# Optimization experiments

Measured on AMD Instinct MI355X. Metric: run time of the kernel, lower is better.

## Reference

```python
import jax, jax.numpy as jnp
import numpy as np

B, S, D, H, T = 64, 512, 1024, 1024, 9


def setup_inputs() -> dict:
    key = jax.random.key(0)
    ks = jax.random.split(key, 8)
    return {
        "input_": jax.random.normal(ks[0], (B, S, D), dtype=jnp.float32),
        "labels": jax.random.randint(ks[1], (B, S), 0, T),
        "attention_mask": jnp.ones((B, S), dtype=jnp.int32),
        # linear_1: input_dim -> hidden_dim (stored [in, out])
        "W1": (jax.random.normal(ks[2], (D, H), dtype=jnp.float32) * 0.02),
        "b1": jnp.zeros((H,), dtype=jnp.float32),
        # linear_2: hidden_dim -> tag_dim
        "W2": (jax.random.normal(ks[3], (H, T), dtype=jnp.float32) * 0.02),
        "b2": jnp.zeros((T,), dtype=jnp.float32),
        # torchcrf params: uniform(-0.1, 0.1)
        "start_trans": jax.random.uniform(ks[4], (T,), minval=-0.1, maxval=0.1),
        "end_trans": jax.random.uniform(ks[5], (T,), minval=-0.1, maxval=0.1),
        "trans": jax.random.uniform(ks[6], (T, T), minval=-0.1, maxval=0.1),
    }


def _crf_mean_llh(logits, tags, mask, start, end, trans):
    """torchcrf.CRF log-likelihood, reduction='mean'. logits [B,S,T]."""
    nb = logits.shape[0]
    em = jnp.transpose(logits, (1, 0, 2))          # [S,B,T] time-major
    tg = tags.T                                    # [S,B]
    m = mask.T.astype(logits.dtype)                # [S,B]
    bidx = jnp.arange(nb)

    # --- numerator: score of the gold path ---
    score0 = start[tg[0]] + em[0, bidx, tg[0]]

    def num_step(carry, x):
        score, last = carry
        em_t, tag_t, m_t = x
        score = score + (trans[last, tag_t] + em_t[bidx, tag_t]) * m_t
        last = jnp.where(m_t > 0, tag_t, last)
        return (score, last), None

    (score, last), _ = jax.lax.scan(num_step, (score0, tg[0]), (em[1:], tg[1:], m[1:]))
    score = score + end[last]

    # --- denominator: log-partition via logsumexp forward recurrence ---
    alpha0 = start[None, :] + em[0]                # [B,T]

    def part_step(alpha, x):
        em_t, m_t = x
        # [B, prev T, next T] semiring (log-sum-exp) matrix product
        nxt = jax.nn.logsumexp(alpha[:, :, None] + trans[None, :, :] + em_t[:, None, :], axis=1)
        alpha = jnp.where(m_t[:, None] > 0, nxt, alpha)
        return alpha, None

    alpha, _ = jax.lax.scan(part_step, alpha0, (em[1:], m[1:]))
    log_z = jax.nn.logsumexp(alpha + end[None, :], axis=1)

    return jnp.mean(score - log_z)


def reference(input_, labels, attention_mask, W1, b1, W2, b2, start_trans, end_trans, trans):
    # dropout layers are identity in eval mode
    h = input_ @ W1 + b1                           # [B,S,H]
    logits = h @ W2 + b2                           # [B,S,T]
    llh = _crf_mean_llh(logits, labels, attention_mask, start_trans, end_trans, trans)
    loss = -llh                                    # forward returns (-1*crf_llh, logits)
    return (loss, logits)
```

## Files before the change

### kernel.cpp

```cpp
#include <hip/hip_runtime.h>

#define BD 64
#define SD 512
#define DD 1024
#define HD 1024
#define TD 9
#define NSEG 8
#define SEGL 64
#define NEGI -1e30f

__device__ __forceinline__ float lse9(const float v[9]) {
    float m0 = fmaxf(v[0], v[1]);
    float m1 = fmaxf(v[2], v[3]);
    float m2 = fmaxf(v[4], v[5]);
    float m3 = fmaxf(v[6], v[7]);
    float mx = fmaxf(fmaxf(m0, m1), fmaxf(fmaxf(m2, m3), v[8]));
    float s = __expf(v[0] - mx) + __expf(v[1] - mx) + __expf(v[2] - mx)
            + __expf(v[3] - mx) + __expf(v[4] - mx) + __expf(v[5] - mx)
            + __expf(v[6] - mx) + __expf(v[7] - mx) + __expf(v[8] - mx);
    return mx + __logf(s);
}

__global__ __launch_bounds__(256) void k_w12(const float* __restrict__ W1,
                                             const float* __restrict__ b1,
                                             const float* __restrict__ W2,
                                             const float* __restrict__ b2,
                                             float* __restrict__ W12t,
                                             float* __restrict__ b12) {
    __shared__ float sh_w2[HD * TD];
    __shared__ float red[256 * TD];
    const int tid = threadIdx.x;
    const int d = blockIdx.x;

    for (int i = tid; i < HD * TD / 4; i += 256)
        ((float4*)sh_w2)[i] = ((const float4*)W2)[i];
    __syncthreads();

    const float* row = (d < DD) ? (W1 + (size_t)d * HD) : b1;
    float4 x = ((const float4*)row)[tid];

    float acc[TD];
#pragma unroll
    for (int t = 0; t < TD; t++) acc[t] = 0.f;
#pragma unroll
    for (int u = 0; u < 4; u++) {
        float xv = (&x.x)[u];
        int h = tid * 4 + u;
#pragma unroll
        for (int t = 0; t < TD; t++) acc[t] += xv * sh_w2[h * TD + t];
    }
#pragma unroll
    for (int t = 0; t < TD; t++) red[tid * TD + t] = acc[t];
    __syncthreads();

    if (tid < TD) {
        float s = 0.f;
        for (int i = 0; i < 256; i++) s += red[i * TD + tid];
        if (d < DD) W12t[tid * DD + d] = s;
        else        b12[tid] = s + b2[tid];
    }
}

__global__ __launch_bounds__(256) void k_gemm2(const float* __restrict__ X,
                                               const float* __restrict__ W12t,
                                               const float* __restrict__ b12,
                                               float* __restrict__ logits) {
    __shared__ float wt[TD][DD];
    __shared__ float bb[TD];

    for (int i = threadIdx.x; i < TD * DD / 4; i += 256)
        ((float4*)&wt[0][0])[i] = ((const float4*)W12t)[i];
    if (threadIdx.x < TD) bb[threadIdx.x] = b12[threadIdx.x];
    __syncthreads();

    const int wave = threadIdx.x >> 6;
    const int lane = threadIdx.x & 63;
    const int g = lane >> 3;
    const int l8 = lane & 7;
    const int row = blockIdx.x * 32 + wave * 8 + g;

    const float4* xr = (const float4*)(X + (size_t)row * DD);

    float acc[TD];
#pragma unroll
    for (int t = 0; t < TD; t++) acc[t] = 0.f;

#pragma unroll 4
    for (int k = 0; k < 32; k++) {
        int d4 = l8 + k * 8;
        float4 x = xr[d4];
#pragma unroll
        for (int t = 0; t < TD; t++) {
            float4 w = *(const float4*)&wt[t][d4 * 4];
            acc[t] += x.x * w.x + x.y * w.y + x.z * w.z + x.w * w.w;
        }
    }

#pragma unroll
    for (int t = 0; t < TD; t++) {
        float v = acc[t];
        v += __shfl_xor(v, 1);
        v += __shfl_xor(v, 2);
        v += __shfl_xor(v, 4);
        acc[t] = v;
    }

    float* out = logits + (size_t)row * TD;
    if (l8 < 8) out[l8] = acc[l8] + bb[l8];
    if (l8 == 0) out[8] = acc[8] + bb[8];
}

__global__ __launch_bounds__(256) void k_crf_seg(const float* __restrict__ logits,
                                                 const int* __restrict__ maskp,
                                                 const float* __restrict__ transp,
                                                 float* __restrict__ segP) {
    const int blk = blockIdx.x;
    const int b = blk >> 3, s = blk & 7;
    const int tid = threadIdx.x;

    __shared__ float tr[81];
    __shared__ float em[SEGL * 9];
    __shared__ int   mk[SEGL];
    __shared__ float bufA[32 * 81];
    __shared__ float bufB[16 * 81];

    const int t0 = s * SEGL + 1;

    for (int i = tid; i < SEGL * 9; i += 256) {
        int q = i / 9, j = i - q * 9;
        int t = t0 + q;
        em[i] = (t < SD) ? logits[((size_t)b * SD + t) * TD + j] : 0.f;
    }
    if (tid < SEGL) {
        int t = t0 + tid;
        mk[tid] = (t < SD) ? maskp[b * SD + t] : 0;
    }
    if (tid < 81) tr[tid] = transp[tid];
    __syncthreads();

    for (int e = tid; e < 32 * 81; e += 256) {
        int p = e / 81, r = e - p * 81;
        int i = r / 9, j = r - i * 9;
        int la = 2 * p, lb = 2 * p + 1;
        int mA = mk[la], mB = mk[lb];
        float out;
        if (mA && mB) {
            float v[9];
#pragma unroll
            for (int k = 0; k < 9; k++)
                v[k] = tr[i * 9 + k] + em[la * 9 + k] + tr[k * 9 + j];
            out = lse9(v) + em[lb * 9 + j];
        } else if (mA) {
            out = tr[r] + em[la * 9 + j];
        } else if (mB) {
            out = tr[r] + em[lb * 9 + j];
        } else {
            out = (i == j) ? 0.f : NEGI;
        }
        bufA[e] = out;
    }
    __syncthreads();

#define COMBINE(SRC, DST, NP)                                        \
    for (int e = tid; e < (NP) * 81; e += 256) {                     \
        int p = e / 81, r = e - p * 81;                              \
        int i = r / 9, j = r - i * 9;                                \
        const float* Am = (SRC) + (2 * p) * 81;                      \
        const float* Bm = (SRC) + (2 * p + 1) * 81;                  \
        float v[9];                                                  \
        _Pragma("unroll")                                            \
        for (int k = 0; k < 9; k++) v[k] = Am[i * 9 + k] + Bm[k * 9 + j]; \
        (DST)[e] = lse9(v);                                          \
    }                                                                \
    __syncthreads();

    COMBINE(bufA, bufB, 16)
    COMBINE(bufB, bufA, 8)
    COMBINE(bufA, bufB, 4)
    COMBINE(bufB, bufA, 2)

    if (tid < 81) {
        int i = tid / 9, j = tid - (tid / 9) * 9;
        float v[9];
#pragma unroll
        for (int k = 0; k < 9; k++) v[k] = bufA[i * 9 + k] + bufA[81 + k * 9 + j];
        segP[(size_t)blk * 81 + tid] = lse9(v);
    }
}

__global__ __launch_bounds__(256) void k_crf_fin(const float* __restrict__ logits,
                                                 const int* __restrict__ labels,
                                                 const int* __restrict__ maskp,
                                                 const float* __restrict__ startp,
                                                 const float* __restrict__ endp,
                                                 const float* __restrict__ transp,
                                                 const float* __restrict__ segP,
                                                 float* __restrict__ diff) {
    const int b = blockIdx.x;
    const int tid = threadIdx.x;

    __shared__ float S[8 * 81];
    __shared__ float A4[4 * 81];
    __shared__ float A2[2 * 81];
    __shared__ float P[81];
    __shared__ float finv[81];
    __shared__ float red[256];
    __shared__ int   redi[256];

    for (int i = tid; i < 8 * 81; i += 256) S[i] = segP[(size_t)b * 8 * 81 + i];
    __syncthreads();

    for (int e = tid; e < 4 * 81; e += 256) {
        int p = e / 81, r = e - p * 81;
        int i = r / 9, j = r - i * 9;
        const float* Am = S + (2 * p) * 81;
        const float* Bm = S + (2 * p + 1) * 81;
        float v[9];
#pragma unroll
        for (int k = 0; k < 9; k++) v[k] = Am[i * 9 + k] + Bm[k * 9 + j];
        A4[e] = lse9(v);
    }
    __syncthreads();

    for (int e = tid; e < 2 * 81; e += 256) {
        int p = e / 81, r = e - p * 81;
        int i = r / 9, j = r - i * 9;
        const float* Am = A4 + (2 * p) * 81;
        const float* Bm = A4 + (2 * p + 1) * 81;
        float v[9];
#pragma unroll
        for (int k = 0; k < 9; k++) v[k] = Am[i * 9 + k] + Bm[k * 9 + j];
        A2[e] = lse9(v);
    }
    __syncthreads();

    if (tid < 81) {
        int i = tid / 9, j = tid - (tid / 9) * 9;
        float v[9];
#pragma unroll
        for (int k = 0; k < 9; k++) v[k] = A2[i * 9 + k] + A2[81 + k * 9 + j];
        P[tid] = lse9(v);
    }
    __syncthreads();

    if (tid < 81) {
        int k = tid / 9, j = tid - (tid / 9) * 9;
        finv[tid] = startp[k] + logits[(size_t)b * SD * TD + k] + P[tid] + endp[j];
    }

    float part = 0.f;
    for (int t = 1 + tid; t < SD; t += 256) {
        if (maskp[b * SD + t]) {
            int tgp = labels[b * SD + t - 1];
            int tgc = labels[b * SD + t];
            part += transp[tgp * TD + tgc] + logits[((size_t)b * SD + t) * TD + tgc];
        }
    }
    int lastt = 0;
    for (int t = tid; t < SD; t += 256) {
        if (maskp[b * SD + t]) lastt = max(lastt, t);
    }
    red[tid] = part;
    redi[tid] = lastt;
    __syncthreads();

    if (tid < 64) {
        float p4 = red[tid] + red[tid + 64] + red[tid + 128] + red[tid + 192];
        int l4 = max(max(redi[tid], redi[tid + 64]), max(redi[tid + 128], redi[tid + 192]));
#pragma unroll
        for (int m = 1; m < 64; m <<= 1) {
            p4 += __shfl_xor(p4, m);
            l4 = max(l4, __shfl_xor(l4, m));
        }
        float v1 = finv[tid];
        float v2 = (tid + 64 < 81) ? finv[tid + 64] : NEGI;
        float mx = fmaxf(v1, v2);
#pragma unroll
        for (int m = 1; m < 64; m <<= 1) mx = fmaxf(mx, __shfl_xor(mx, m));
        float ssum = __expf(v1 - mx) + __expf(v2 - mx);
#pragma unroll
        for (int m = 1; m < 64; m <<= 1) ssum += __shfl_xor(ssum, m);
        float logz = mx + __logf(ssum);

        if (tid == 0) {
            int tg0 = labels[b * SD];
            int tgl = labels[b * SD + l4];
            float score = p4 + startp[tg0] + logits[(size_t)b * SD * TD + tg0] + endp[tgl];
            diff[b] = score - logz;
        }
    }
}

__global__ __launch_bounds__(64) void k_loss(const float* __restrict__ diff,
                                             float* __restrict__ out) {
    float v = (threadIdx.x < BD) ? diff[threadIdx.x] : 0.f;
#pragma unroll
    for (int m = 1; m < 64; m <<= 1) v += __shfl_xor(v, m);
    if (threadIdx.x == 0) out[0] = -v / (float)BD;
}

extern "C" void kernel_launch(void* const* d_in, const int* in_sizes, int n_in,
                              void* d_out, int out_size, void* d_ws, size_t ws_size,
                              hipStream_t stream) {
    const float* X      = (const float*)d_in[0];
    const int*   labels = (const int*)d_in[1];
    const int*   maskp  = (const int*)d_in[2];
    const float* W1     = (const float*)d_in[3];
    const float* b1     = (const float*)d_in[4];
    const float* W2     = (const float*)d_in[5];
    const float* b2     = (const float*)d_in[6];
    const float* startp = (const float*)d_in[7];
    const float* endp   = (const float*)d_in[8];
    const float* transp = (const float*)d_in[9];

    float* out = (float*)d_out;
    float* ws = (float*)d_ws;

    float* diff = ws;
    float* W12t = ws + 64;
    float* b12  = ws + 64 + DD * TD;
    float* segP = ws + 64 + DD * TD + 16;
    float* logits = out + 1;

    hipLaunchKernelGGL(k_w12, dim3(DD + 1), dim3(256), 0, stream,
                       W1, b1, W2, b2, W12t, b12);
    hipLaunchKernelGGL(k_gemm2, dim3(BD * SD / 32), dim3(256), 0, stream,
                       X, W12t, b12, logits);
    hipLaunchKernelGGL(k_crf_seg, dim3(BD * NSEG), dim3(256), 0, stream,
                       logits, maskp, transp, segP);
    hipLaunchKernelGGL(k_crf_fin, dim3(BD), dim3(256), 0, stream,
                       logits, labels, maskp, startp, endp, transp, segP, diff);
    hipLaunchKernelGGL(k_loss, dim3(1), dim3(64), 0, stream, diff, out);
}
```

Baseline: 61.48 us.

## Fuse logits GEMV into CRF segment kernel and batch W1·W2 rows per block

The logits projection and the CRF segment-scan kernel are merged into one kernel: each block computes logits for its 64-step segment plus one boundary row, writes them to global memory, and keeps emissions in shared memory for the semiring scan. This drops a launch and the global round trip of logits into the CRF kernel. The shared buffer used for W12 is reused afterwards for the scan buffers. Separately, the W1·W2 precompute now handles 8 rows per block using wave shuffle reductions instead of one row per block with a serial shared-memory reduction. The trade-off is that the fused kernel has only 512 blocks, fewer than the previous GEMV launch had, and each block recomputes one boundary row.

```diff
diff --git a/kernel.cpp b/kernel.cpp
--- a/kernel.cpp
+++ b/kernel.cpp
@@ -28,115 +28,128 @@
                                              float* __restrict__ W12t,
                                              float* __restrict__ b12) {
     __shared__ float sh_w2[HD * TD];
-    __shared__ float red[256 * TD];
+    __shared__ float wred[4][TD];
     const int tid = threadIdx.x;
-    const int d = blockIdx.x;
+    const int wave = tid >> 6, lane = tid & 63;
 
     for (int i = tid; i < HD * TD / 4; i += 256)
         ((float4*)sh_w2)[i] = ((const float4*)W2)[i];
     __syncthreads();
 
-    const float* row = (d < DD) ? (W1 + (size_t)d * HD) : b1;
-    float4 x = ((const float4*)row)[tid];
-
-    float acc[TD];
-#pragma unroll
-    for (int t = 0; t < TD; t++) acc[t] = 0.f;
-#pragma unroll
-    for (int u = 0; u < 4; u++) {
-        float xv = (&x.x)[u];
-        int h = tid * 4 + u;
-#pragma unroll
-        for (int t = 0; t < TD; t++) acc[t] += xv * sh_w2[h * TD + t];
-    }
-#pragma unroll
-    for (int t = 0; t < TD; t++) red[tid * TD + t] = acc[t];
-    __syncthreads();
-
-    if (tid < TD) {
-        float s = 0.f;
-        for (int i = 0; i < 256; i++) s += red[i * TD + tid];
-        if (d < DD) W12t[tid * DD + d] = s;
-        else        b12[tid] = s + b2[tid];
-    }
-}
-
-__global__ __launch_bounds__(256) void k_gemm2(const float* __restrict__ X,
+    for (int rr = 0; rr < 8; rr++) {
+        int d = blockIdx.x * 8 + rr;
+        if (d > DD) break;
+        const float* row = (d < DD) ? (W1 + (size_t)d * HD) : b1;
+        float4 x = ((const float4*)row)[tid];
+
+        float acc[TD];
+#pragma unroll
+        for (int t = 0; t < TD; t++) acc[t] = 0.f;
+#pragma unroll
+        for (int u = 0; u < 4; u++) {
+            float xv = (&x.x)[u];
+            int h = tid * 4 + u;
+#pragma unroll
+            for (int t = 0; t < TD; t++) acc[t] += xv * sh_w2[h * TD + t];
+        }
+#pragma unroll
+        for (int t = 0; t < TD; t++) {
+            float v = acc[t];
+#pragma unroll
+            for (int m = 1; m < 64; m <<= 1) v += __shfl_xor(v, m);
+            acc[t] = v;
+        }
+        if (lane == 0) {
+#pragma unroll
+            for (int t = 0; t < TD; t++) wred[wave][t] = acc[t];
+        }
+        __syncthreads();
+        if (tid < TD) {
+            float s = wred[0][tid] + wred[1][tid] + wred[2][tid] + wred[3][tid];
+            if (d < DD) W12t[tid * DD + d] = s;
+            else        b12[tid] = s + b2[tid];
+        }
+        __syncthreads();
+    }
+}
+
+__global__ __launch_bounds__(256) void k_fused(const float* __restrict__ X,
                                                const float* __restrict__ W12t,
                                                const float* __restrict__ b12,
-                                               float* __restrict__ logits) {
-    __shared__ float wt[TD][DD];
+                                               const int* __restrict__ maskp,
+                                               const float* __restrict__ transp,
+                                               float* __restrict__ logits,
+                                               float* __restrict__ segP) {
+    __shared__ float smem[TD * DD];
+    __shared__ float em[SEGL * TD];
+    __shared__ int   mk[SEGL];
+    __shared__ float tr[81];
     __shared__ float bb[TD];
 
-    for (int i = threadIdx.x; i < TD * DD / 4; i += 256)
-        ((float4*)&wt[0][0])[i] = ((const float4*)W12t)[i];
-    if (threadIdx.x < TD) bb[threadIdx.x] = b12[threadIdx.x];
-    __syncthreads();
-
-    const int wave = threadIdx.x >> 6;
-    const int lane = threadIdx.x & 63;
-    const int g = lane >> 3;
-    const int l8 = lane & 7;
-    const int row = blockIdx.x * 32 + wave * 8 + g;
-
-    const float4* xr = (const float4*)(X + (size_t)row * DD);
-
-    float acc[TD];
-#pragma unroll
-    for (int t = 0; t < TD; t++) acc[t] = 0.f;
-
-#pragma unroll 4
-    for (int k = 0; k < 32; k++) {
-        int d4 = l8 + k * 8;
-        float4 x = xr[d4];
-#pragma unroll
-        for (int t = 0; t < TD; t++) {
-            float4 w = *(const float4*)&wt[t][d4 * 4];
-            acc[t] += x.x * w.x + x.y * w.y + x.z * w.z + x.w * w.w;
-        }
-    }
-
-#pragma unroll
-    for (int t = 0; t < TD; t++) {
-        float v = acc[t];
-        v += __shfl_xor(v, 1);
-        v += __shfl_xor(v, 2);
-        v += __shfl_xor(v, 4);
-        acc[t] = v;
-    }
-
-    float* out = logits + (size_t)row * TD;
-    if (l8 < 8) out[l8] = acc[l8] + bb[l8];
-    if (l8 == 0) out[8] = acc[8] + bb[8];
-}
-
-__global__ __launch_bounds__(256) void k_crf_seg(const float* __restrict__ logits,
-                                                 const int* __restrict__ maskp,
-                                                 const float* __restrict__ transp,
-                                                 float* __restrict__ segP) {
     const int blk = blockIdx.x;
     const int b = blk >> 3, s = blk & 7;
     const int tid = threadIdx.x;
-
-    __shared__ float tr[81];
-    __shared__ float em[SEGL * 9];
-    __shared__ int   mk[SEGL];
-    __shared__ float bufA[32 * 81];
-    __shared__ float bufB[16 * 81];
-
-    const int t0 = s * SEGL + 1;
-
-    for (int i = tid; i < SEGL * 9; i += 256) {
-        int q = i / 9, j = i - q * 9;
-        int t = t0 + q;
-        em[i] = (t < SD) ? logits[((size_t)b * SD + t) * TD + j] : 0.f;
-    }
+    const int wave = tid >> 6, lane = tid & 63;
+    const int g = lane >> 3, l8 = lane & 7;
+    const int t0 = s * SEGL;
+
+    for (int i = tid; i < TD * DD / 4; i += 256)
+        ((float4*)smem)[i] = ((const float4*)W12t)[i];
+    if (tid < TD) bb[tid] = b12[tid];
+    if (tid < 81) tr[tid] = transp[tid];
     if (tid < SEGL) {
-        int t = t0 + tid;
+        int t = t0 + 1 + tid;
         mk[tid] = (t < SD) ? maskp[b * SD + t] : 0;
     }
-    if (tid < 81) tr[tid] = transp[tid];
-    __syncthreads();
+    __syncthreads();
+
+    for (int grp = wave; grp < 9; grp += 4) {
+        int rr = grp * 8 + g;
+        int gr = t0 + rr;
+        bool valid = (rr <= SEGL) && (gr < SD);
+
+        float acc[TD];
+#pragma unroll
+        for (int t = 0; t < TD; t++) acc[t] = 0.f;
+        if (valid) {
+            const float4* xr = (const float4*)(X + ((size_t)b * SD + gr) * DD);
+#pragma unroll 4
+            for (int k = 0; k < 32; k++) {
+                int d4 = l8 + k * 8;
+                float4 x = xr[d4];
+#pragma unroll
+                for (int t = 0; t < TD; t++) {
+                    const float4 w = *(const float4*)&smem[t * DD + d4 * 4];
+                    acc[t] += x.x * w.x + x.y * w.y + x.z * w.z + x.w * w.w;
+                }
+            }
+        }
+#pragma unroll
+        for (int t = 0; t < TD; t++) {
+            float v = acc[t];
+            v += __shfl_xor(v, 1);
+            v += __shfl_xor(v, 2);
+            v += __shfl_xor(v, 4);
+            acc[t] = v;
+        }
+        if (valid) {
+            float v0 = acc[l8] + bb[l8];
+            float v8 = acc[8] + bb[8];
+            if (rr < SEGL) {
+                float* orow = logits + ((size_t)b * SD + gr) * TD;
+                orow[l8] = v0;
+                if (l8 == 0) orow[8] = v8;
+            }
+            if (rr >= 1) {
+                em[(rr - 1) * TD + l8] = v0;
+                if (l8 == 0) em[(rr - 1) * TD + 8] = v8;
+            }
+        }
+    }
+    __syncthreads();
+
+    float* bufA = smem;
+    float* bufB = smem + 32 * 81;
 
     for (int e = tid; e < 32 * 81; e += 256) {
         int p = e / 81, r = e - p * 81;
@@ -322,12 +335,10 @@
     float* segP = ws + 64 + DD * TD + 16;
     float* logits = out + 1;
 
-    hipLaunchKernelGGL(k_w12, dim3(DD + 1), dim3(256), 0, stream,
+    hipLaunchKernelGGL(k_w12, dim3(129), dim3(256), 0, stream,
                        W1, b1, W2, b2, W12t, b12);
-    hipLaunchKernelGGL(k_gemm2, dim3(BD * SD / 32), dim3(256), 0, stream,
-                       X, W12t, b12, logits);
-    hipLaunchKernelGGL(k_crf_seg, dim3(BD * NSEG), dim3(256), 0, stream,
-                       logits, maskp, transp, segP);
+    hipLaunchKernelGGL(k_fused, dim3(BD * NSEG), dim3(256), 0, stream,
+                       X, W12t, b12, maskp, transp, logits, segP);
     hipLaunchKernelGGL(k_crf_fin, dim3(BD), dim3(256), 0, stream,
                        logits, labels, maskp, startp, endp, transp, segP, diff);
     hipLaunchKernelGGL(k_loss, dim3(1), dim3(64), 0, stream, diff, out);
```

Measured after the change: 90.06 us. +46.5%, slower.
